# Optimization experiments

Hardware: AMD Instinct MI355X
Metric: run time of the kernel (lower is better)

Reference implementation:

```python
import jax, jax.numpy as jnp
import numpy as np

N_NODES = 100000
N_EDGES = 1600000
IN_DIM = 128
LATENT = [128, 128, 16]  # last entry = num classes (logits dim)


def setup_inputs() -> dict:
    key = jax.random.key(0)
    ks = jax.random.split(key, 16)
    inp = {
        "x": jax.random.normal(ks[0], (N_NODES, IN_DIM), dtype=jnp.float32),
        "edge_index": jax.random.randint(ks[1], (2, N_EDGES), 0, N_NODES, dtype=jnp.int64),
        "edge_weight": jax.random.uniform(ks[2], (N_EDGES,), dtype=jnp.float32),
    }
    dims = [IN_DIM] + LATENT
    for i in range(len(LATENT)):
        fan_in = dims[i]
        scale = 1.0 / np.sqrt(fan_in)
        inp[f"W{i}"] = jax.random.uniform(ks[3 + 2 * i], (dims[i], dims[i + 1]), minval=-scale, maxval=scale, dtype=jnp.float32)
        inp[f"b{i}"] = jax.random.uniform(ks[4 + 2 * i], (dims[i + 1],), minval=-scale, maxval=scale, dtype=jnp.float32)
        inp[f"eps{i}"] = jnp.zeros((), dtype=jnp.float32)  # GINConv train_eps init = 0
    return inp


def _gin_layer(x, W, b, eps, src, dst, edge_weight):
    # message: x_j (optionally scaled by edge weight), summed into target nodes
    msg = x[src]
    if edge_weight is not None:
        msg = msg * edge_weight[:, None]
    agg = jax.ops.segment_sum(msg, dst, num_segments=N_NODES)
    h = (1.0 + eps) * x + agg
    return jax.nn.relu(h @ W + b)  # MLP = Linear + ReLU


def _l2_normalize(x, eps=1e-12):
    norm = jnp.linalg.norm(x, axis=-1, keepdims=True)
    return x / jnp.maximum(norm, eps)


def reference(x, edge_index, edge_weight, W0, b0, eps0, W1, b1, eps1, W2, b2, eps2):
    src, dst = edge_index[0], edge_index[1]
    params = [(W0, b0, eps0), (W1, b1, eps1), (W2, b2, eps2)]
    h = x
    # all but last layer: GINConv(with edge_weight) -> l2 normalize -> ReLU
    for (W, b, e) in params[:-1]:
        h = _gin_layer(h, W, b, e, src, dst, edge_weight)
        h = _l2_normalize(h)  # emb_normlize=True
        h = jax.nn.relu(h)
    # last layer: GINConv WITHOUT edge_weight (forward passes only x, edge_index)
    W, b, e = params[-1]
    logits = _gin_layer(h, W, b, e, src, dst, None)
    probs = jax.nn.softmax(logits, axis=-1)
    return (logits, probs)
```

## Files before the change

### kernel.cpp

```cpp
#include <hip/hip_runtime.h>
#include <hip/hip_bf16.h>

#define N_NODES 100000
#define N_EDGES 1600000
#define DIM 128
#define ODIM 16
#define NB 782
#define PCHUNK 3200
#define PBLK 500
#define FCAP 2560
#define CAST1 3125
#define CAST2 3125

typedef unsigned int uint32;
typedef float f32x2 __attribute__((ext_vector_type(2)));
typedef float f32x4 __attribute__((ext_vector_type(4)));
typedef short bf16x8 __attribute__((ext_vector_type(8)));
typedef uint32 u32x4 __attribute__((ext_vector_type(4)));
typedef uint32 u32x2 __attribute__((ext_vector_type(2)));

#define W15_INV (1.0f / 32767.0f)

static __device__ __forceinline__ float bflo(uint32 p) { return __uint_as_float(p << 16); }
static __device__ __forceinline__ float bfhi(uint32 p) { return __uint_as_float(p & 0xFFFF0000u); }
static __device__ __forceinline__ unsigned short f2bf(float f) {
  __hip_bfloat16 h = __float2bfloat16(f);
  return *reinterpret_cast<unsigned short*>(&h);
}
static __device__ __forceinline__ uint32 pk2bf(float a, float b) {
  return (uint32)f2bf(a) | ((uint32)f2bf(b) << 16);
}

__global__ __launch_bounds__(512) void prep_part_kernel(
    const int* __restrict__ src, const int* __restrict__ dst,
    const float* __restrict__ ew, int* __restrict__ bcur,
    int2* __restrict__ epack2,
    const f32x4* __restrict__ x4, uint32* __restrict__ Xu,
    const float* __restrict__ W0, const float* __restrict__ W1,
    const float* __restrict__ W2,
    unsigned short* __restrict__ pW0, unsigned short* __restrict__ pW1,
    unsigned short* __restrict__ pW2) {
  int b = blockIdx.x;
  int tid = threadIdx.x;
  if (b < PBLK) {
    __shared__ int hist[NB];
    __shared__ int base_a[NB];
    __shared__ int lcur_a[NB];
    __shared__ int gbase_a[NB];
    __shared__ int2 stg[PCHUNK];
    __shared__ int gpos[PCHUNK];

    int e0 = b * PCHUNK;

    for (int i = tid; i < NB; i += 512) hist[i] = 0;
    __syncthreads();
    for (int i = tid; i < PCHUNK; i += 512) atomicAdd(&hist[dst[e0 + i] >> 7], 1);
    __syncthreads();

    if (tid < 64) {
      int run = 0;
#pragma unroll
      for (int c = 0; c < 13; c++) {
        int idx = c * 64 + tid;
        int v = (idx < NB) ? hist[idx] : 0;
        int incl = v;
#pragma unroll
        for (int off = 1; off < 64; off <<= 1) {
          int t1 = __shfl_up(incl, off, 64);
          if (tid >= off) incl += t1;
        }
        if (idx < NB) base_a[idx] = run + incl - v;
        run += __shfl(incl, 63, 64);
      }
    }
    __syncthreads();
    for (int i = tid; i < NB; i += 512) {
      int c = hist[i];
      gbase_a[i] = (c > 0) ? i * FCAP + atomicAdd(&bcur[i], c) : 0;
      lcur_a[i] = base_a[i];
    }
    __syncthreads();

    for (int i = tid; i < PCHUNK; i += 512) {
      int e = e0 + i;
      int s = __builtin_nontemporal_load(src + e);
      int d = dst[e];
      float w = __builtin_nontemporal_load(ew + e);
      int bkt = d >> 7;
      int pos = atomicAdd(&lcur_a[bkt], 1);
      stg[pos] = make_int2(s | ((d & 127) << 20), __float_as_int(w));
      gpos[pos] = gbase_a[bkt] + (pos - base_a[bkt]);
    }
    __syncthreads();
    for (int i = tid; i < PCHUNK; i += 512) epack2[gpos[i]] = stg[i];
  } else if (b < PBLK + CAST1) {
    int i = (b - PBLK) * 512 + tid;
    f32x4 v = __builtin_nontemporal_load(x4 + i);
    u32x2 o = {pk2bf(v[0], v[1]), pk2bf(v[2], v[3])};
    *(u32x2*)(Xu + (size_t)i * 2) = o;
  } else if (b < PBLK + CAST1 + 64) {
    int bb = b - PBLK - CAST1;
    int wsel = bb >> 5;
    int idx = (bb & 31) * 512 + tid;
    int j = idx & 7, lane = (idx >> 3) & 63, nt = (idx >> 9) & 7, kc = idx >> 12;
    const float* W = wsel ? W1 : W0;
    unsigned short* pW = wsel ? pW1 : pW0;
    pW[idx] = f2bf(W[(kc * 32 + (lane >> 4) * 8 + j) * DIM + nt * 16 + (lane & 15)]);
  } else {
    int idx = (b - PBLK - CAST1 - 64) * 512 + tid;
    int j = idx & 7, lane = (idx >> 3) & 63, kc = idx >> 9;
    pW2[idx] = f2bf(W2[(kc * 32 + (lane >> 4) * 8 + j) * ODIM + (lane & 15)]);
  }
}

__global__ __launch_bounds__(512) void sort_cast_kernel(
    const int* __restrict__ bcur, const int2* __restrict__ epack2,
    uint32* __restrict__ ep4, int* __restrict__ row_ptr,
    int* __restrict__ row_end,
    const f32x4* __restrict__ x4, uint32* __restrict__ Xu) {
  int b = blockIdx.x;
  int tid = threadIdx.x;
  if (b < NB) {
    __shared__ int2 ebuf[FCAP];
    __shared__ unsigned short inv[FCAP];
    __shared__ int hist[128];
    __shared__ int sc[128];
    __shared__ int cur[128];
    int node0 = b << 7;
    int lo = b * FCAP;

    if (tid < 128) hist[tid] = 0;
    __syncthreads();
    int n = bcur[b];
    if (n > FCAP) n = FCAP;

    for (int i = tid; i < n; i += 512) {
      int2 e = epack2[lo + i];
      ebuf[i] = e;
      atomicAdd(&hist[(e.x >> 20) & 127], 1);
    }
    __syncthreads();
    if (tid < 64) {
      int run = 0;
#pragma unroll
      for (int c = 0; c < 2; c++) {
        int idx = c * 64 + tid;
        int v = hist[idx];
        int incl = v;
#pragma unroll
        for (int off = 1; off < 64; off <<= 1) {
          int tv = __shfl_up(incl, off, 64);
          if (tid >= off) incl += tv;
        }
        sc[idx] = run + incl;
        run += __shfl(incl, 63, 64);
      }
    }
    __syncthreads();
    if (tid < 128) {
      int node = node0 + tid;
      if (node < N_NODES) {
        row_ptr[node] = lo + sc[tid] - hist[tid];
        row_end[node] = lo + sc[tid];
      }
      cur[tid] = sc[tid] - hist[tid];
    }
    __syncthreads();
    for (int i = tid; i < n; i += 512) {
      int p = atomicAdd(&cur[(ebuf[i].x >> 20) & 127], 1);
      inv[p] = (unsigned short)i;
    }
    __syncthreads();
    for (int p = tid; p < n; p += 512) {
      int2 e = ebuf[inv[p]];
      uint32 w15 = __float2uint_rn(__int_as_float(e.y) * 32767.0f);
      ep4[lo + p] = ((uint32)e.x & 0x1FFFFu) | (w15 << 17);
    }
  } else {
    int i = (CAST1 + (b - NB)) * 512 + tid;
    f32x4 v = __builtin_nontemporal_load(x4 + i);
    u32x2 o = {pk2bf(v[0], v[1]), pk2bf(v[2], v[3])};
    *(u32x2*)(Xu + (size_t)i * 2) = o;
  }
}

__global__ __launch_bounds__(256, 8) void gather_bf16(
    const uint32* __restrict__ hu, const int* __restrict__ row_ptr,
    const int* __restrict__ row_end, const uint32* __restrict__ ep,
    const float* __restrict__ eps_p, uint32* __restrict__ cg) {
  int lane = threadIdx.x & 63;
  int node = blockIdx.x * 4 + (threadIdx.x >> 6);
  if (node >= N_NODES) return;
  int grp = lane >> 4, l4 = lane & 15;
  int a = row_ptr[node], bnd = row_end[node];
  float epf = 1.0f + *eps_p;
  uint4 xv = *(const uint4*)(hu + (size_t)node * 64 + l4 * 4);
  f32x2 acc2[4];
#pragma unroll
  for (int k = 0; k < 4; k++) acc2[k] = (f32x2){0.f, 0.f};

  auto acc8 = [&](float wv, const uint4& p) {
    acc2[0] += (f32x2){bflo(p.x), bfhi(p.x)} * wv;
    acc2[1] += (f32x2){bflo(p.y), bfhi(p.y)} * wv;
    acc2[2] += (f32x2){bflo(p.z), bfhi(p.z)} * wv;
    acc2[3] += (f32x2){bflo(p.w), bfhi(p.w)} * wv;
  };

#pragma unroll 2
  for (int j = a; j < bnd; j += 16) {
    int i0 = j + grp;
    int i1 = i0 + 4;
    int i2 = i0 + 8;
    int i3 = i0 + 12;
    uint32 e0 = ep[i0 < bnd ? i0 : a];
    uint32 e1 = ep[i1 < bnd ? i1 : a];
    uint32 e2 = ep[i2 < bnd ? i2 : a];
    uint32 e3 = ep[i3 < bnd ? i3 : a];
    uint4 p0 = *(const uint4*)(hu + (size_t)(e0 & 0x1FFFFu) * 64 + l4 * 4);
    uint4 p1 = *(const uint4*)(hu + (size_t)(e1 & 0x1FFFFu) * 64 + l4 * 4);
    uint4 p2 = *(const uint4*)(hu + (size_t)(e2 & 0x1FFFFu) * 64 + l4 * 4);
    uint4 p3 = *(const uint4*)(hu + (size_t)(e3 & 0x1FFFFu) * 64 + l4 * 4);
    float w0 = i0 < bnd ? (float)(e0 >> 17) * W15_INV : 0.f;
    float w1 = i1 < bnd ? (float)(e1 >> 17) * W15_INV : 0.f;
    float w2 = i2 < bnd ? (float)(e2 >> 17) * W15_INV : 0.f;
    float w3 = i3 < bnd ? (float)(e3 >> 17) * W15_INV : 0.f;
    acc8(w0, p0);
    acc8(w1, p1);
    acc8(w2, p2);
    acc8(w3, p3);
  }
#pragma unroll
  for (int k = 0; k < 4; k++) {
    acc2[k].x += __shfl_xor(acc2[k].x, 16, 64);
    acc2[k].x += __shfl_xor(acc2[k].x, 32, 64);
    acc2[k].y += __shfl_xor(acc2[k].y, 16, 64);
    acc2[k].y += __shfl_xor(acc2[k].y, 32, 64);
  }
  if (lane < 16) {
    u32x4 st;
    st[0] = pk2bf(fmaf(epf, bflo(xv.x), acc2[0].x), fmaf(epf, bfhi(xv.x), acc2[0].y));
    st[1] = pk2bf(fmaf(epf, bflo(xv.y), acc2[1].x), fmaf(epf, bfhi(xv.y), acc2[1].y));
    st[2] = pk2bf(fmaf(epf, bflo(xv.z), acc2[2].x), fmaf(epf, bfhi(xv.z), acc2[2].y));
    st[3] = pk2bf(fmaf(epf, bflo(xv.w), acc2[3].x), fmaf(epf, bfhi(xv.w), acc2[3].y));
    __builtin_nontemporal_store(st, (u32x4*)(cg + (size_t)node * 64 + l4 * 4));
  }
}

template <int FUSE_PROJ>
__global__ __launch_bounds__(256) void gin_mlp_mfma(
    const uint32* __restrict__ Cu,
    const unsigned char* __restrict__ pW, const float* __restrict__ b,
    uint32* outH, const unsigned char* __restrict__ pW2,
    uint32* __restrict__ yb) {
  __shared__ __align__(16) unsigned char As[64 * 272];
  int tid = threadIdx.x;
  int node0 = blockIdx.x * 64;

  const uint4* C4 = (const uint4*)Cu;
#pragma unroll
  for (int c = 0; c < 4; c++) {
    int t = c * 256 + tid;
    int n = t >> 4, s = t & 15;
    int node = node0 + n;
    int cn = node < N_NODES ? node : N_NODES - 1;
    *(uint4*)(As + n * 272 + s * 16) = C4[(size_t)cn * 16 + s];
  }
  __syncthreads();

  int w = tid >> 6, l = tid & 63;
  int m = l & 15, q = l >> 4;

  f32x4 acc[8];
#pragma unroll
  for (int nt = 0; nt < 8; nt++) acc[nt] = (f32x4){0.f, 0.f, 0.f, 0.f};

  const unsigned char* Abase = As + (w * 16 + m) * 272 + q * 16;
#pragma unroll
  for (int kc = 0; kc < 4; kc++) {
    bf16x8 af = *(const bf16x8*)(Abase + kc * 64);
#pragma unroll
    for (int nt = 0; nt < 8; nt++) {
      bf16x8 bfr = *(const bf16x8*)(pW + (size_t)((kc * 8 + nt) * 64 + l) * 16);
      acc[nt] = __builtin_amdgcn_mfma_f32_16x16x32_bf16(af, bfr, acc[nt], 0, 0, 0);
    }
  }

  float ss[4] = {0.f, 0.f, 0.f, 0.f};
#pragma unroll
  for (int nt = 0; nt < 8; nt++) {
    float bj = b[nt * 16 + m];
#pragma unroll
    for (int r = 0; r < 4; r++) {
      float v = fmaxf(acc[nt][r] + bj, 0.0f);
      acc[nt][r] = v;
      ss[r] += v * v;
    }
  }
#pragma unroll
  for (int r = 0; r < 4; r++) {
    float s = ss[r];
    s += __shfl_xor(s, 1, 64);
    s += __shfl_xor(s, 2, 64);
    s += __shfl_xor(s, 4, 64);
    s += __shfl_xor(s, 8, 64);
    ss[r] = 1.0f / fmaxf(sqrtf(s), 1e-12f);
  }
#pragma unroll
  for (int nt = 0; nt < 8; nt++) {
#pragma unroll
    for (int r = 0; r < 4; r++) {
      unsigned short hv = f2bf(acc[nt][r] * ss[r]);
      *(unsigned short*)(As + (w * 16 + q * 4 + r) * 272 + (nt * 16 + m) * 2) = hv;
    }
  }

  if (FUSE_PROJ) {
    f32x4 accy = (f32x4){0.f, 0.f, 0.f, 0.f};
#pragma unroll
    for (int kc = 0; kc < 4; kc++) {
      bf16x8 af = *(const bf16x8*)(Abase + kc * 64);
      bf16x8 bfr = *(const bf16x8*)(pW2 + (size_t)(kc * 64 + l) * 16);
      accy = __builtin_amdgcn_mfma_f32_16x16x32_bf16(af, bfr, accy, 0, 0, 0);
    }
#pragma unroll
    for (int r = 0; r < 4; r++) {
      float v = accy[r];
      float o = __shfl_xor(v, 1, 64);
      if (!(m & 1)) {
        int orow = node0 + w * 16 + q * 4 + r;
        if (orow < N_NODES) yb[(size_t)orow * 8 + (m >> 1)] = pk2bf(v, o);
      }
    }
  } else {
    __syncthreads();
    int rem = N_NODES - node0; if (rem > 64) rem = 64;
    for (int i = tid; i < 1024; i += 256) {
      int row = i >> 4, seg = i & 15;
      if (row < rem) {
        uint4 vv = *(const uint4*)(As + row * 272 + seg * 16);
        *(uint4*)((unsigned char*)outH + (size_t)(node0 + row) * 256 + seg * 16) = vv;
      }
    }
  }
}

__global__ __launch_bounds__(256) void gather16_final_kernel(
    const uint32* __restrict__ yb, const int* __restrict__ row_ptr,
    const int* __restrict__ row_end, const uint32* __restrict__ ep,
    const float* __restrict__ bb, const float* __restrict__ eps_p,
    float* __restrict__ out_logits, float* __restrict__ out_probs) {
  int lane = threadIdx.x & 63;
  int node = blockIdx.x * 4 + (threadIdx.x >> 6);
  if (node >= N_NODES) return;
  int f2 = lane & 3;
  int eq = lane >> 2;
  int a = row_ptr[node], bnd = row_end[node];
  f32x4 acc = (f32x4){0.f, 0.f, 0.f, 0.f};
  for (int j = a; j < bnd; j += 16) {
    int idx = j + eq;
    int vld = idx < bnd;
    uint32 e = ep[vld ? idx : a];
    u32x2 p = *(const u32x2*)(yb + (size_t)(e & 0x1FFFFu) * 8 + f2 * 2);
    if (vld) {
      acc[0] += bflo(p[0]); acc[1] += bfhi(p[0]);
      acc[2] += bflo(p[1]); acc[3] += bfhi(p[1]);
    }
  }
#pragma unroll
  for (int k = 0; k < 4; k++) {
#pragma unroll
    for (int off = 4; off <= 32; off <<= 1)
      acc[k] += __shfl_xor(acc[k], off, 64);
  }
  if (eq == 0) {
    float epf = 1.0f + *eps_p;
    u32x2 ys = *(const u32x2*)(yb + (size_t)node * 8 + f2 * 2);
    f32x4 lg;
    lg[0] = fmaxf(fmaf(epf, bflo(ys[0]), acc[0]) + bb[f2 * 4 + 0], 0.f);
    lg[1] = fmaxf(fmaf(epf, bfhi(ys[0]), acc[1]) + bb[f2 * 4 + 1], 0.f);
    lg[2] = fmaxf(fmaf(epf, bflo(ys[1]), acc[2]) + bb[f2 * 4 + 2], 0.f);
    lg[3] = fmaxf(fmaf(epf, bfhi(ys[1]), acc[3]) + bb[f2 * 4 + 3], 0.f);
    float mx = fmaxf(fmaxf(lg[0], lg[1]), fmaxf(lg[2], lg[3]));
    mx = fmaxf(mx, __shfl_xor(mx, 1, 4));
    mx = fmaxf(mx, __shfl_xor(mx, 2, 4));
    f32x4 ex;
    float s = 0.f;
#pragma unroll
    for (int k = 0; k < 4; k++) { ex[k] = __expf(lg[k] - mx); s += ex[k]; }
    s += __shfl_xor(s, 1, 4);
    s += __shfl_xor(s, 2, 4);
    float invs = 1.0f / s;
    size_t base = (size_t)node * ODIM + f2 * 4;
    *(f32x4*)(out_logits + base) = lg;
    f32x4 pr = {ex[0] * invs, ex[1] * invs, ex[2] * invs, ex[3] * invs};
    *(f32x4*)(out_probs + base) = pr;
  }
}

extern "C" void kernel_launch(void* const* d_in, const int* in_sizes, int n_in,
                              void* d_out, int out_size, void* d_ws, size_t ws_size,
                              hipStream_t stream) {
  const float* x = (const float*)d_in[0];
  const int* ei = (const int*)d_in[1];
  const float* ew = (const float*)d_in[2];
  const float* W0 = (const float*)d_in[3];
  const float* b0 = (const float*)d_in[4];
  const float* e0 = (const float*)d_in[5];
  const float* W1 = (const float*)d_in[6];
  const float* b1 = (const float*)d_in[7];
  const float* e1 = (const float*)d_in[8];
  const float* W2 = (const float*)d_in[9];
  const float* b2 = (const float*)d_in[10];
  const float* e2 = (const float*)d_in[11];
  float* out = (float*)d_out;

  const int* srcp = ei;
  const int* dstp = ei + N_EDGES;

  char* ws = (char*)d_ws;
  size_t off = 0;
  uint32* Cg  = (uint32*)(ws + off);  off += (size_t)N_NODES * DIM * 2;
  int2* epack2 = (int2*)Cg;
  uint32* Xb  = (uint32*)(ws + off);  off += (size_t)N_NODES * DIM * 2;
  uint32* H   = (uint32*)(ws + off);  off += (size_t)N_NODES * DIM * 2;
  uint32* ep4 = (uint32*)(ws + off);  off += (size_t)NB * FCAP * 4 + 4096;
  uint32* yb  = (uint32*)(ws + off);  off += (size_t)N_NODES * 8 * 4;
  int* row_ptr = (int*)(ws + off);    off += (size_t)(N_NODES + 16) * 4;
  int* row_end = (int*)(ws + off);    off += (size_t)(N_NODES + 16) * 4;
  int* bcur   = (int*)(ws + off);     off += 4096;
  unsigned short* pW0 = (unsigned short*)(ws + off); off += 32768;
  unsigned short* pW1 = (unsigned short*)(ws + off); off += 32768;
  unsigned short* pW2 = (unsigned short*)(ws + off); off += 4096;

  hipMemsetAsync(bcur, 0, 4096, stream);
  prep_part_kernel<<<PBLK + CAST1 + 64 + 4, 512, 0, stream>>>(
      srcp, dstp, ew, bcur, epack2,
      (const f32x4*)x, Xb, W0, W1, W2, pW0, pW1, pW2);

  sort_cast_kernel<<<NB + CAST2, 512, 0, stream>>>(
      bcur, epack2, ep4, row_ptr, row_end, (const f32x4*)x, Xb);

  int ggrid = (N_NODES + 3) / 4;
  int mgrid = (N_NODES + 63) / 64;

  gather_bf16<<<ggrid, 256, 0, stream>>>(Xb, row_ptr, row_end, ep4, e0, Cg);
  gin_mlp_mfma<0><<<mgrid, 256, 0, stream>>>(Cg, (const unsigned char*)pW0, b0,
                                             H, nullptr, nullptr);
  gather_bf16<<<ggrid, 256, 0, stream>>>(H, row_ptr, row_end, ep4, e1, Cg);
  gin_mlp_mfma<1><<<mgrid, 256, 0, stream>>>(Cg, (const unsigned char*)pW1, b1,
                                             nullptr, (const unsigned char*)pW2, yb);
  gather16_final_kernel<<<ggrid, 256, 0, stream>>>(yb, row_ptr, row_end, ep4,
                                                   b2, e2, out,
                                                   out + (size_t)N_NODES * ODIM);
}
```

Baseline: 333.7 us.

## Pack edge weight early and split partition buffer into word and byte arrays

The partition stage now quantizes the edge weight to 15 bits and packs it with the source index before scattering. It writes a 4-byte word plus a 1-byte local-destination array instead of 8-byte pairs, which cuts partition scatter and sort read traffic and drops the gpos shared array. The partition chunk grows to 4000 edges over 400 blocks, and the MLP output store becomes nontemporal. Byte-granular scattered stores may coalesce poorly, and the larger shared staging can lower occupancy.

Measured after the change: 334.9 us. No clear change (+0.4%).

```diff
diff --git a/kernel.cpp b/kernel.cpp
--- a/kernel.cpp
+++ b/kernel.cpp
@@ -6,8 +6,8 @@
 #define DIM 128
 #define ODIM 16
 #define NB 782
-#define PCHUNK 3200
-#define PBLK 500
+#define PCHUNK 4000
+#define PBLK 400
 #define FCAP 2560
 #define CAST1 3125
 #define CAST2 3125
@@ -34,7 +34,7 @@
 __global__ __launch_bounds__(512) void prep_part_kernel(
     const int* __restrict__ src, const int* __restrict__ dst,
     const float* __restrict__ ew, int* __restrict__ bcur,
-    int2* __restrict__ epack2,
+    uint32* __restrict__ epX, unsigned char* __restrict__ epD,
     const f32x4* __restrict__ x4, uint32* __restrict__ Xu,
     const float* __restrict__ W0, const float* __restrict__ W1,
     const float* __restrict__ W2,
@@ -48,7 +48,6 @@
     __shared__ int lcur_a[NB];
     __shared__ int gbase_a[NB];
     __shared__ int2 stg[PCHUNK];
-    __shared__ int gpos[PCHUNK];
 
     int e0 = b * PCHUNK;
 
@@ -86,13 +85,18 @@
       int s = __builtin_nontemporal_load(src + e);
       int d = dst[e];
       float w = __builtin_nontemporal_load(ew + e);
-      int bkt = d >> 7;
-      int pos = atomicAdd(&lcur_a[bkt], 1);
-      stg[pos] = make_int2(s | ((d & 127) << 20), __float_as_int(w));
-      gpos[pos] = gbase_a[bkt] + (pos - base_a[bkt]);
-    }
-    __syncthreads();
-    for (int i = tid; i < PCHUNK; i += 512) epack2[gpos[i]] = stg[i];
+      uint32 w15 = __float2uint_rn(w * 32767.0f);
+      int pos = atomicAdd(&lcur_a[d >> 7], 1);
+      stg[pos] = make_int2((int)(((uint32)s) | (w15 << 17)), d);
+    }
+    __syncthreads();
+    for (int i = tid; i < PCHUNK; i += 512) {
+      int2 e = stg[i];
+      int bkt = e.y >> 7;
+      int gp = gbase_a[bkt] + (i - base_a[bkt]);
+      epX[gp] = (uint32)e.x;
+      epD[gp] = (unsigned char)(e.y & 127);
+    }
   } else if (b < PBLK + CAST1) {
     int i = (b - PBLK) * 512 + tid;
     f32x4 v = __builtin_nontemporal_load(x4 + i);
@@ -114,14 +118,16 @@
 }
 
 __global__ __launch_bounds__(512) void sort_cast_kernel(
-    const int* __restrict__ bcur, const int2* __restrict__ epack2,
+    const int* __restrict__ bcur, const uint32* __restrict__ epX,
+    const unsigned char* __restrict__ epD,
     uint32* __restrict__ ep4, int* __restrict__ row_ptr,
     int* __restrict__ row_end,
     const f32x4* __restrict__ x4, uint32* __restrict__ Xu) {
   int b = blockIdx.x;
   int tid = threadIdx.x;
   if (b < NB) {
-    __shared__ int2 ebuf[FCAP];
+    __shared__ uint32 ebuf[FCAP];
+    __shared__ unsigned char dbuf[FCAP];
     __shared__ unsigned short inv[FCAP];
     __shared__ int hist[128];
     __shared__ int sc[128];
@@ -135,9 +141,10 @@
     if (n > FCAP) n = FCAP;
 
     for (int i = tid; i < n; i += 512) {
-      int2 e = epack2[lo + i];
-      ebuf[i] = e;
-      atomicAdd(&hist[(e.x >> 20) & 127], 1);
+      ebuf[i] = epX[lo + i];
+      unsigned char d = epD[lo + i];
+      dbuf[i] = d;
+      atomicAdd(&hist[d], 1);
     }
     __syncthreads();
     if (tid < 64) {
@@ -167,15 +174,11 @@
     }
     __syncthreads();
     for (int i = tid; i < n; i += 512) {
-      int p = atomicAdd(&cur[(ebuf[i].x >> 20) & 127], 1);
+      int p = atomicAdd(&cur[dbuf[i]], 1);
       inv[p] = (unsigned short)i;
     }
     __syncthreads();
-    for (int p = tid; p < n; p += 512) {
-      int2 e = ebuf[inv[p]];
-      uint32 w15 = __float2uint_rn(__int_as_float(e.y) * 32767.0f);
-      ep4[lo + p] = ((uint32)e.x & 0x1FFFFu) | (w15 << 17);
-    }
+    for (int p = tid; p < n; p += 512) ep4[lo + p] = ebuf[inv[p]];
   } else {
     int i = (CAST1 + (b - NB)) * 512 + tid;
     f32x4 v = __builtin_nontemporal_load(x4 + i);
@@ -337,8 +340,9 @@
     for (int i = tid; i < 1024; i += 256) {
       int row = i >> 4, seg = i & 15;
       if (row < rem) {
-        uint4 vv = *(const uint4*)(As + row * 272 + seg * 16);
-        *(uint4*)((unsigned char*)outH + (size_t)(node0 + row) * 256 + seg * 16) = vv;
+        u32x4 vv = *(const u32x4*)(As + row * 272 + seg * 16);
+        __builtin_nontemporal_store(
+            vv, (u32x4*)((unsigned char*)outH + (size_t)(node0 + row) * 256 + seg * 16));
       }
     }
   }
@@ -420,7 +424,8 @@
   char* ws = (char*)d_ws;
   size_t off = 0;
   uint32* Cg  = (uint32*)(ws + off);  off += (size_t)N_NODES * DIM * 2;
-  int2* epack2 = (int2*)Cg;
+  uint32* epX = (uint32*)Cg;
+  unsigned char* epD = (unsigned char*)Cg + (size_t)NB * FCAP * 4 + 4096;
   uint32* Xb  = (uint32*)(ws + off);  off += (size_t)N_NODES * DIM * 2;
   uint32* H   = (uint32*)(ws + off);  off += (size_t)N_NODES * DIM * 2;
   uint32* ep4 = (uint32*)(ws + off);  off += (size_t)NB * FCAP * 4 + 4096;
@@ -434,11 +439,11 @@
 
   hipMemsetAsync(bcur, 0, 4096, stream);
   prep_part_kernel<<<PBLK + CAST1 + 64 + 4, 512, 0, stream>>>(
-      srcp, dstp, ew, bcur, epack2,
+      srcp, dstp, ew, bcur, epX, epD,
       (const f32x4*)x, Xb, W0, W1, W2, pW0, pW1, pW2);
 
   sort_cast_kernel<<<NB + CAST2, 512, 0, stream>>>(
-      bcur, epack2, ep4, row_ptr, row_end, (const f32x4*)x, Xb);
+      bcur, epX, epD, ep4, row_ptr, row_end, (const f32x4*)x, Xb);
 
   int ggrid = (N_NODES + 3) / 4;
   int mgrid = (N_NODES + 63) / 64;
```
